# Kernel tuning notes

Measured on AMD Instinct MI355X. Metric: run time of the kernel, lower is better.

The kernel has to match this reference:

```python
import jax, jax.numpy as jnp
import numpy as np
import math

D_K = 64

def setup_inputs() -> dict:
    key = jax.random.key(0)
    k1, k2, k3, k4 = jax.random.split(key, 4)
    B, H, S, D = 2, 16, 2048, D_K
    query = jax.random.normal(k1, (B, H, S, D), dtype=jnp.float32)
    kk = jax.random.normal(k2, (B, H, S, D), dtype=jnp.float32)
    value = jax.random.normal(k3, (B, H, S, D), dtype=jnp.float32)
    mask = jax.random.randint(k4, (B, 1, S, S), 0, 2).astype(bool)
    return {"query": query, "key": kk, "value": value, "mask": mask}

def reference(query, key, value, mask):
    # score = Q K^T / sqrt(d_k)  -> [B,H,S,S]
    score = jnp.einsum('bhqd,bhkd->bhqk', query, key) * (1.0 / math.sqrt(D_K))
    # masked_fill(mask, -inf)
    score = jnp.where(mask, -jnp.inf, score)
    attn = jax.nn.softmax(score, axis=-1)
    # rows that are fully masked produce NaN -> 0 (torch.nan_to_num)
    attn = jnp.nan_to_num(attn, nan=0.0)
    # dropout with drop_rate=0 is identity
    return jnp.einsum('bhqk,bhkd->bhqd', attn, value)
```

## Files before the change

kernel.cpp:

```cpp
#include <hip/hip_runtime.h>
#include <hip/hip_bf16.h>


#define S_LEN 2048
#define D_DIM 64
#define BH    32
#define BM    64
#define BN    64
#define NW    4
#define LDK   72
#define QSCALE 0.1803368801f

typedef __bf16 bf16_t;
typedef bf16_t bf16x8 __attribute__((ext_vector_type(8)));
typedef float  f32x4  __attribute__((ext_vector_type(4)));
typedef unsigned short u16;
typedef unsigned char  u8;
typedef unsigned long long u64b;

template<int CTRL>
__device__ __forceinline__ float dppmov(float v) {
    return __builtin_bit_cast(float,
        __builtin_amdgcn_update_dpp(0, __builtin_bit_cast(int, v),
                                    CTRL, 0xF, 0xF, true));
}
__device__ __forceinline__ float redsum16(float v) {
    v += dppmov<0xB1>(v);
    v += dppmov<0x4E>(v);
    v += dppmov<0x141>(v);
    v += dppmov<0x140>(v);
    return v;
}

__global__ __launch_bounds__(256)
void mask_to_bits(const unsigned* __restrict__ M, u64b* __restrict__ bm)
{
    const int t = threadIdx.x;
    unsigned p = M[(t * 8179) & ((1 << 21) - 1)];
    const int is_u8 = __syncthreads_or(p > 1u);
    const int id = blockIdx.x * 256 + t;
    u64b w = 0;
    if (is_u8) {
        const uint4* src = (const uint4*)((const u8*)M + (size_t)id * 64);
        #pragma unroll
        for (int g = 0; g < 4; ++g) {
            uint4 x = src[g];
            const unsigned dw[4] = {x.x, x.y, x.z, x.w};
            #pragma unroll
            for (int q = 0; q < 4; ++q) {
                const unsigned v = dw[q];
                const int base = g * 16 + q * 4;
                if (v & 0x000000FFu) w |= 1ull << (base + 0);
                if (v & 0x0000FF00u) w |= 1ull << (base + 1);
                if (v & 0x00FF0000u) w |= 1ull << (base + 2);
                if (v & 0xFF000000u) w |= 1ull << (base + 3);
            }
        }
    } else {
        const uint4* src = (const uint4*)(M + (size_t)id * 64);
        #pragma unroll
        for (int g = 0; g < 16; ++g) {
            uint4 x = src[g];
            if (x.x) w |= 1ull << (g * 4 + 0);
            if (x.y) w |= 1ull << (g * 4 + 1);
            if (x.z) w |= 1ull << (g * 4 + 2);
            if (x.w) w |= 1ull << (g * 4 + 3);
        }
    }
    bm[id] = w;
}

__global__ __launch_bounds__(256)
void k_to_bf16(const float* __restrict__ K, bf16_t* __restrict__ Kb)
{
    const size_t i = ((size_t)blockIdx.x * 256 + threadIdx.x) * 8;
    float4 a = *(const float4*)(K + i);
    float4 b = *(const float4*)(K + i + 4);
    bf16x8 w;
    w[0]=(bf16_t)a.x; w[1]=(bf16_t)a.y; w[2]=(bf16_t)a.z; w[3]=(bf16_t)a.w;
    w[4]=(bf16_t)b.x; w[5]=(bf16_t)b.y; w[6]=(bf16_t)b.z; w[7]=(bf16_t)b.w;
    *(bf16x8*)(Kb + i) = w;
}

__global__ __launch_bounds__(256)
void v_transpose(const float* __restrict__ V, bf16_t* __restrict__ Vt)
{
    __shared__ bf16_t T[128][LDK];
    const int t  = threadIdx.x;
    const int sc = blockIdx.x;
    const int bh = blockIdx.y;
    const float* Vh = V + ((size_t)bh * S_LEN + sc * 128) * D_DIM;
    #pragma unroll
    for (int it = 0; it < 4; ++it) {
        const int row = it * 32 + (t >> 3);
        const int c8  = (t & 7) * 8;
        float4 a = *(const float4*)(Vh + row * D_DIM + c8);
        float4 b = *(const float4*)(Vh + row * D_DIM + c8 + 4);
        bf16_t* d = &T[row][c8];
        d[0]=(bf16_t)a.x; d[1]=(bf16_t)a.y; d[2]=(bf16_t)a.z; d[3]=(bf16_t)a.w;
        d[4]=(bf16_t)b.x; d[5]=(bf16_t)b.y; d[6]=(bf16_t)b.z; d[7]=(bf16_t)b.w;
    }
    __syncthreads();
    bf16_t* out = Vt + ((size_t)bh * D_DIM + (t >> 2)) * S_LEN
                     + (size_t)sc * 128 + (t & 3) * 32;
    #pragma unroll
    for (int g = 0; g < 4; ++g) {
        bf16x8 w;
        #pragma unroll
        for (int j = 0; j < 8; ++j) w[j] = T[(t & 3) * 32 + g * 8 + j][t >> 2];
        *(bf16x8*)(out + g * 8) = w;
    }
}

__global__ __launch_bounds__(256, 4)
void fa_fwd(const float* __restrict__ Q, const float* __restrict__ K,
            const float* __restrict__ V, const void* __restrict__ M,
            const u64b* __restrict__ bm, const bf16_t* __restrict__ Kb,
            const bf16_t* __restrict__ Vt, float* __restrict__ O)
{
    __shared__ __align__(16) bf16_t Klds[BN * LDK];
    __shared__ __align__(16) bf16_t Vtlds[D_DIM * LDK];
    __shared__ __align__(16) bf16_t Plds[NW][16 * LDK];

    const int tid  = threadIdx.x;
    const int wave = tid >> 6;
    const int lane = tid & 63;
    const int quad = lane >> 4;
    const int ln   = lane & 15;

    const int qt = blockIdx.x;
    const int bh = blockIdx.y;
    const int b  = bh >> 4;

    const int qbase = qt * BM + wave * 16;

    const size_t head_off = (size_t)bh * S_LEN * D_DIM;
    const float* Qh = Q + head_off;
    const float* Kh = K + head_off;
    const float* Vh = V + head_off;
    const bf16_t* Kbh = Kb ? (Kb + head_off) : nullptr;
    const bf16_t* Vth = Vt ? (Vt + head_off) : nullptr;
    const u8*  Mb8  = (const u8*)M  + (size_t)b * S_LEN * S_LEN;
    const int* Mb32 = (const int*)M + (size_t)b * S_LEN * S_LEN;

    int mask_is_u8 = 0;
    if (!bm) {
        int probe = ((const int*)M)[(tid * 8179) & ((1 << 21) - 1)];
        mask_is_u8 = __syncthreads_or((unsigned)probe > 1u);
    }

    bf16x8 qfrag[2];
    {
        const float* qrow = Qh + (size_t)(qbase + ln) * D_DIM;
        #pragma unroll
        for (int s = 0; s < 2; ++s) {
            float4 a = *(const float4*)(qrow + s * 32 + quad * 8);
            float4 c = *(const float4*)(qrow + s * 32 + quad * 8 + 4);
            bf16x8 w;
            w[0] = (bf16_t)(a.x * QSCALE); w[1] = (bf16_t)(a.y * QSCALE);
            w[2] = (bf16_t)(a.z * QSCALE); w[3] = (bf16_t)(a.w * QSCALE);
            w[4] = (bf16_t)(c.x * QSCALE); w[5] = (bf16_t)(c.y * QSCALE);
            w[6] = (bf16_t)(c.z * QSCALE); w[7] = (bf16_t)(c.w * QSCALE);
            qfrag[s] = w;
        }
    }

    f32x4 accO[4] = {{0.f,0.f,0.f,0.f},{0.f,0.f,0.f,0.f},
                     {0.f,0.f,0.f,0.f},{0.f,0.f,0.f,0.f}};
    float lpart[4] = {0.f, 0.f, 0.f, 0.f};

    const int srow = tid >> 2;
    const int sgrp = tid & 3;
    const int crow = tid >> 3;
    const int cc8  = (tid & 7) * 8;

    const size_t bmrow_base = ((size_t)b * S_LEN + qbase + quad * 4) * 32;

    for (int kb = 0; kb < S_LEN; kb += BN) {
        __syncthreads();

        if (Kbh) {
            #pragma unroll
            for (int it = 0; it < 2; ++it) {
                const int row = it * 32 + crow;
                bf16x8 wk = *(const bf16x8*)(Kbh + (size_t)(kb + row) * D_DIM + cc8);
                *(bf16x8*)&Klds[row * LDK + cc8] = wk;
                bf16x8 wv = *(const bf16x8*)(Vth + (size_t)row * S_LEN + kb + cc8);
                *(bf16x8*)&Vtlds[row * LDK + cc8] = wv;
            }
        } else {
            const float* kp = Kh + (size_t)(kb + srow) * D_DIM + sgrp * 16;
            #pragma unroll
            for (int h = 0; h < 2; ++h) {
                float4 a = *(const float4*)(kp + h * 8);
                float4 c = *(const float4*)(kp + h * 8 + 4);
                bf16x8 w;
                w[0] = (bf16_t)a.x; w[1] = (bf16_t)a.y;
                w[2] = (bf16_t)a.z; w[3] = (bf16_t)a.w;
                w[4] = (bf16_t)c.x; w[5] = (bf16_t)c.y;
                w[6] = (bf16_t)c.z; w[7] = (bf16_t)c.w;
                *(bf16x8*)&Klds[srow * LDK + sgrp * 16 + h * 8] = w;
            }
            const float* vp = Vh + (size_t)(kb + srow) * D_DIM + sgrp * 16;
            float vv[16];
            #pragma unroll
            for (int g = 0; g < 4; ++g) {
                float4 a = *(const float4*)(vp + g * 4);
                vv[g*4+0] = a.x; vv[g*4+1] = a.y;
                vv[g*4+2] = a.z; vv[g*4+3] = a.w;
            }
            #pragma unroll
            for (int jj = 0; jj < 16; ++jj) {
                const int j = (jj + srow) & 15;
                Vtlds[(sgrp * 16 + j) * LDK + srow] = (bf16_t)vv[j];
            }
        }
        __syncthreads();

        f32x4 Sacc[4] = {{0.f,0.f,0.f,0.f},{0.f,0.f,0.f,0.f},
                         {0.f,0.f,0.f,0.f},{0.f,0.f,0.f,0.f}};
        #pragma unroll
        for (int s = 0; s < 2; ++s) {
            #pragma unroll
            for (int t = 0; t < 4; ++t) {
                bf16x8 bk = *(const bf16x8*)&Klds[(16*t + ln) * LDK + s*32 + quad*8];
                Sacc[t] = __builtin_amdgcn_mfma_f32_16x16x32_bf16(qfrag[s], bk, Sacc[t], 0, 0, 0);
            }
        }

        #pragma unroll
        for (int r = 0; r < 4; ++r) {
            float ps[4];
            if (bm) {
                const u64b w  = bm[bmrow_base + (size_t)r * 32 + (kb >> 6)];
                const u64b wl = w >> ln;
                ps[0] = ( wl        & 1ull) ? 0.f : __builtin_amdgcn_exp2f(Sacc[0][r]);
                ps[1] = ((wl >> 16) & 1ull) ? 0.f : __builtin_amdgcn_exp2f(Sacc[1][r]);
                ps[2] = ((wl >> 32) & 1ull) ? 0.f : __builtin_amdgcn_exp2f(Sacc[2][r]);
                ps[3] = ((wl >> 48) & 1ull) ? 0.f : __builtin_amdgcn_exp2f(Sacc[3][r]);
            } else if (mask_is_u8) {
                const u8* mp = Mb8 + (size_t)(qbase + quad*4 + r) * S_LEN + kb + ln;
                #pragma unroll
                for (int t = 0; t < 4; ++t)
                    ps[t] = mp[16*t] ? 0.f : __builtin_amdgcn_exp2f(Sacc[t][r]);
            } else {
                const int* mp = Mb32 + (size_t)(qbase + quad*4 + r) * S_LEN + kb + ln;
                #pragma unroll
                for (int t = 0; t < 4; ++t)
                    ps[t] = mp[16*t] ? 0.f : __builtin_amdgcn_exp2f(Sacc[t][r]);
            }
            lpart[r] += (ps[0] + ps[1]) + (ps[2] + ps[3]);
            #pragma unroll
            for (int t = 0; t < 4; ++t)
                Plds[wave][(quad*4 + r) * LDK + 16*t + ln] = (bf16_t)ps[t];
        }

        __asm__ volatile("" ::: "memory");

        #pragma unroll
        for (int s2 = 0; s2 < 2; ++s2) {
            bf16x8 pa = *(const bf16x8*)&Plds[wave][ln * LDK + s2*32 + quad*8];
            #pragma unroll
            for (int dt = 0; dt < 4; ++dt) {
                bf16x8 bv = *(const bf16x8*)&Vtlds[(16*dt + ln) * LDK + s2*32 + quad*8];
                accO[dt] = __builtin_amdgcn_mfma_f32_16x16x32_bf16(pa, bv, accO[dt], 0, 0, 0);
            }
        }
    }

    #pragma unroll
    for (int r = 0; r < 4; ++r) {
        const float l = redsum16(lpart[r]);
        const float inv = (l > 0.f) ? 1.f / l : 0.f;
        float* orow = O + head_off + (size_t)(qbase + quad*4 + r) * D_DIM;
        #pragma unroll
        for (int dt = 0; dt < 4; ++dt)
            orow[16*dt + ln] = accO[dt][r] * inv;
    }
}

extern "C" void kernel_launch(void* const* d_in, const int* in_sizes, int n_in,
                              void* d_out, int out_size, void* d_ws, size_t ws_size,
                              hipStream_t stream) {
    (void)in_sizes; (void)n_in; (void)out_size;
    const float* Q = (const float*)d_in[0];
    const float* K = (const float*)d_in[1];
    const float* V = (const float*)d_in[2];
    const void*  M = d_in[3];
    float* O = (float*)d_out;

    const size_t bm_bytes = (size_t)2 * S_LEN * (S_LEN / 64) * 8;
    const size_t kv_elems = (size_t)BH * S_LEN * D_DIM;
    const size_t need_kv  = bm_bytes + 2 * kv_elems * sizeof(bf16_t);

    u64b*   bm = (ws_size >= bm_bytes) ? (u64b*)d_ws : nullptr;
    bf16_t* Kb = nullptr;
    bf16_t* Vt = nullptr;
    if (ws_size >= need_kv) {
        Kb = (bf16_t*)((char*)d_ws + bm_bytes);
        Vt = Kb + kv_elems;
    }

    if (bm)
        mask_to_bits<<<dim3(131072 / 256), dim3(256), 0, stream>>>(
            (const unsigned*)M, bm);
    if (Kb) {
        k_to_bf16<<<dim3((unsigned)(kv_elems / 8 / 256)), dim3(256), 0, stream>>>(K, Kb);
        v_transpose<<<dim3(S_LEN / 128, BH), dim3(256), 0, stream>>>(V, Vt);
    }

    dim3 grid(S_LEN / BM, BH);
    fa_fwd<<<grid, dim3(256), 0, stream>>>(Q, K, V, M, bm, Kb, Vt, O);
}
```

Before: 199.0 us.

## Double-buffer K/V tiles via async global-to-LDS loads with XOR-swizzled layout

```diff
diff --git a/kernel.cpp b/kernel.cpp
--- a/kernel.cpp
+++ b/kernel.cpp
@@ -8,7 +8,7 @@
 #define BM    64
 #define BN    64
 #define NW    4
-#define LDK   72
+#define PST   72
 #define QSCALE 0.1803368801f
 
 typedef __bf16 bf16_t;
@@ -17,6 +17,12 @@
 typedef unsigned short u16;
 typedef unsigned char  u8;
 typedef unsigned long long u64b;
+
+__device__ __forceinline__ void load_lds16(const bf16_t* g, bf16_t* l) {
+    __builtin_amdgcn_global_load_lds(
+        (const __attribute__((address_space(1))) void*)g,
+        (__attribute__((address_space(3))) void*)l, 16, 0, 0);
+}
 
 template<int CTRL>
 __device__ __forceinline__ float dppmov(float v) {
@@ -71,21 +77,36 @@
 }
 
 __global__ __launch_bounds__(256)
-void k_to_bf16(const float* __restrict__ K, bf16_t* __restrict__ Kb)
+void qk_prep(const float* __restrict__ Q, const float* __restrict__ K,
+             bf16_t* __restrict__ Qb, bf16_t* __restrict__ Kb)
 {
     const size_t i = ((size_t)blockIdx.x * 256 + threadIdx.x) * 8;
-    float4 a = *(const float4*)(K + i);
-    float4 b = *(const float4*)(K + i + 4);
-    bf16x8 w;
-    w[0]=(bf16_t)a.x; w[1]=(bf16_t)a.y; w[2]=(bf16_t)a.z; w[3]=(bf16_t)a.w;
-    w[4]=(bf16_t)b.x; w[5]=(bf16_t)b.y; w[6]=(bf16_t)b.z; w[7]=(bf16_t)b.w;
-    *(bf16x8*)(Kb + i) = w;
+    {
+        float4 a = *(const float4*)(Q + i);
+        float4 b = *(const float4*)(Q + i + 4);
+        bf16x8 w;
+        w[0]=(bf16_t)(a.x*QSCALE); w[1]=(bf16_t)(a.y*QSCALE);
+        w[2]=(bf16_t)(a.z*QSCALE); w[3]=(bf16_t)(a.w*QSCALE);
+        w[4]=(bf16_t)(b.x*QSCALE); w[5]=(bf16_t)(b.y*QSCALE);
+        w[6]=(bf16_t)(b.z*QSCALE); w[7]=(bf16_t)(b.w*QSCALE);
+        *(bf16x8*)(Qb + i) = w;
+    }
+    {
+        float4 a = *(const float4*)(K + i);
+        float4 b = *(const float4*)(K + i + 4);
+        bf16x8 w;
+        w[0]=(bf16_t)a.x; w[1]=(bf16_t)a.y; w[2]=(bf16_t)a.z; w[3]=(bf16_t)a.w;
+        w[4]=(bf16_t)b.x; w[5]=(bf16_t)b.y; w[6]=(bf16_t)b.z; w[7]=(bf16_t)b.w;
+        const size_t r = i >> 6;
+        const int    g = (int)((i & 63) >> 3);
+        *(bf16x8*)(Kb + r * 64 + ((g ^ (int)(r & 7)) * 8)) = w;
+    }
 }
 
 __global__ __launch_bounds__(256)
 void v_transpose(const float* __restrict__ V, bf16_t* __restrict__ Vt)
 {
-    __shared__ bf16_t T[128][LDK];
+    __shared__ bf16_t T[128][PST];
     const int t  = threadIdx.x;
     const int sc = blockIdx.x;
     const int bh = blockIdx.y;
@@ -101,26 +122,33 @@
         d[4]=(bf16_t)b.x; d[5]=(bf16_t)b.y; d[6]=(bf16_t)b.z; d[7]=(bf16_t)b.w;
     }
     __syncthreads();
-    bf16_t* out = Vt + ((size_t)bh * D_DIM + (t >> 2)) * S_LEN
-                     + (size_t)sc * 128 + (t & 3) * 32;
+    const int d = t >> 2;
     #pragma unroll
     for (int g = 0; g < 4; ++g) {
+        const int s_off = (t & 3) * 32 + g * 8;
+        const int kbt   = sc * 2 + (s_off >> 6);
+        const int k_in  = s_off & 63;
+        const int gk    = k_in >> 3;
         bf16x8 w;
         #pragma unroll
-        for (int j = 0; j < 8; ++j) w[j] = T[(t & 3) * 32 + g * 8 + j][t >> 2];
-        *(bf16x8*)(out + g * 8) = w;
-    }
-}
-
-__global__ __launch_bounds__(256, 4)
+        for (int j = 0; j < 8; ++j) w[j] = T[s_off + j][d];
+        *(bf16x8*)(Vt + (((size_t)bh * (S_LEN/BN) + kbt) * D_DIM + d) * 64
+                      + ((gk ^ (d & 7)) * 8)) = w;
+    }
+}
+
+__global__ __launch_bounds__(256, 3)
 void fa_fwd(const float* __restrict__ Q, const float* __restrict__ K,
             const float* __restrict__ V, const void* __restrict__ M,
-            const u64b* __restrict__ bm, const bf16_t* __restrict__ Kb,
-            const bf16_t* __restrict__ Vt, float* __restrict__ O)
+            const u64b* __restrict__ bm, const bf16_t* __restrict__ Qb,
+            const bf16_t* __restrict__ Kb, const bf16_t* __restrict__ Vt,
+            float* __restrict__ O)
 {
-    __shared__ __align__(16) bf16_t Klds[BN * LDK];
-    __shared__ __align__(16) bf16_t Vtlds[D_DIM * LDK];
-    __shared__ __align__(16) bf16_t Plds[NW][16 * LDK];
+    __shared__ __align__(16) bf16_t KldsA[BN * D_DIM];
+    __shared__ __align__(16) bf16_t KldsB[BN * D_DIM];
+    __shared__ __align__(16) bf16_t VldsA[D_DIM * BN];
+    __shared__ __align__(16) bf16_t VldsB[D_DIM * BN];
+    __shared__ __align__(16) bf16_t Plds[NW][16 * PST];
 
     const int tid  = threadIdx.x;
     const int wave = tid >> 6;
@@ -131,7 +159,6 @@
     const int qt = blockIdx.x;
     const int bh = blockIdx.y;
     const int b  = bh >> 4;
-
     const int qbase = qt * BM + wave * 16;
 
     const size_t head_off = (size_t)bh * S_LEN * D_DIM;
@@ -139,7 +166,6 @@
     const float* Kh = K + head_off;
     const float* Vh = V + head_off;
     const bf16_t* Kbh = Kb ? (Kb + head_off) : nullptr;
-    const bf16_t* Vth = Vt ? (Vt + head_off) : nullptr;
     const u8*  Mb8  = (const u8*)M  + (size_t)b * S_LEN * S_LEN;
     const int* Mb32 = (const int*)M + (size_t)b * S_LEN * S_LEN;
 
@@ -150,17 +176,21 @@
     }
 
     bf16x8 qfrag[2];
-    {
+    if (Qb) {
+        const bf16_t* qrow = Qb + head_off + (size_t)(qbase + ln) * D_DIM;
+        qfrag[0] = *(const bf16x8*)(qrow + quad * 8);
+        qfrag[1] = *(const bf16x8*)(qrow + 32 + quad * 8);
+    } else {
         const float* qrow = Qh + (size_t)(qbase + ln) * D_DIM;
         #pragma unroll
         for (int s = 0; s < 2; ++s) {
             float4 a = *(const float4*)(qrow + s * 32 + quad * 8);
             float4 c = *(const float4*)(qrow + s * 32 + quad * 8 + 4);
             bf16x8 w;
-            w[0] = (bf16_t)(a.x * QSCALE); w[1] = (bf16_t)(a.y * QSCALE);
-            w[2] = (bf16_t)(a.z * QSCALE); w[3] = (bf16_t)(a.w * QSCALE);
-            w[4] = (bf16_t)(c.x * QSCALE); w[5] = (bf16_t)(c.y * QSCALE);
-            w[6] = (bf16_t)(c.z * QSCALE); w[7] = (bf16_t)(c.w * QSCALE);
+            w[0]=(bf16_t)(a.x*QSCALE); w[1]=(bf16_t)(a.y*QSCALE);
+            w[2]=(bf16_t)(a.z*QSCALE); w[3]=(bf16_t)(a.w*QSCALE);
+            w[4]=(bf16_t)(c.x*QSCALE); w[5]=(bf16_t)(c.y*QSCALE);
+            w[6]=(bf16_t)(c.z*QSCALE); w[7]=(bf16_t)(c.w*QSCALE);
             qfrag[s] = w;
         }
     }
@@ -169,102 +199,133 @@
                      {0.f,0.f,0.f,0.f},{0.f,0.f,0.f,0.f}};
     float lpart[4] = {0.f, 0.f, 0.f, 0.f};
 
-    const int srow = tid >> 2;
-    const int sgrp = tid & 3;
-    const int crow = tid >> 3;
-    const int cc8  = (tid & 7) * 8;
-
     const size_t bmrow_base = ((size_t)b * S_LEN + qbase + quad * 4) * 32;
-
-    for (int kb = 0; kb < S_LEN; kb += BN) {
-        __syncthreads();
-
-        if (Kbh) {
-            #pragma unroll
-            for (int it = 0; it < 2; ++it) {
-                const int row = it * 32 + crow;
-                bf16x8 wk = *(const bf16x8*)(Kbh + (size_t)(kb + row) * D_DIM + cc8);
-                *(bf16x8*)&Klds[row * LDK + cc8] = wk;
-                bf16x8 wv = *(const bf16x8*)(Vth + (size_t)row * S_LEN + kb + cc8);
-                *(bf16x8*)&Vtlds[row * LDK + cc8] = wv;
+    const int xg = ln & 7;
+
+    auto load_wm = [&](int kb, u64b* wm) {
+        if (bm) {
+            #pragma unroll
+            for (int r = 0; r < 4; ++r)
+                wm[r] = bm[bmrow_base + (size_t)r * 32 + (kb >> 6)];
+        } else if (mask_is_u8) {
+            #pragma unroll
+            for (int r = 0; r < 4; ++r) {
+                const u8* mp = Mb8 + (size_t)(qbase + quad*4 + r) * S_LEN + kb + ln;
+                u64b w = 0;
+                #pragma unroll
+                for (int t = 0; t < 4; ++t)
+                    if (mp[16*t]) w |= 1ull << (16*t + ln);
+                wm[r] = w;
             }
         } else {
+            #pragma unroll
+            for (int r = 0; r < 4; ++r) {
+                const int* mp = Mb32 + (size_t)(qbase + quad*4 + r) * S_LEN + kb + ln;
+                u64b w = 0;
+                #pragma unroll
+                for (int t = 0; t < 4; ++t)
+                    if (mp[16*t]) w |= 1ull << (16*t + ln);
+                wm[r] = w;
+            }
+        }
+    };
+
+    auto prefetch = [&](int kb, bf16_t* Kl, bf16_t* Vl) {
+        const bf16_t* kt = Kbh + (size_t)kb * D_DIM;
+        const bf16_t* vt = Vt + ((size_t)bh * (S_LEN/BN) + (kb >> 6)) * (BN * D_DIM);
+        #pragma unroll
+        for (int i = 0; i < 2; ++i) {
+            const int c = wave + 4 * i;
+            load_lds16(kt + c * 512 + lane * 8, Kl + c * 512);
+            load_lds16(vt + c * 512 + lane * 8, Vl + c * 512);
+        }
+    };
+
+    auto compute_tile = [&](const bf16_t* Kl, const bf16_t* Vl, const u64b* wm) {
+        f32x4 Sacc[4] = {{0.f,0.f,0.f,0.f},{0.f,0.f,0.f,0.f},
+                         {0.f,0.f,0.f,0.f},{0.f,0.f,0.f,0.f}};
+        #pragma unroll
+        for (int s = 0; s < 2; ++s) {
+            #pragma unroll
+            for (int t = 0; t < 4; ++t) {
+                bf16x8 bk = *(const bf16x8*)
+                    &Kl[(16*t + ln) * D_DIM + (((s*4 + quad) ^ xg) * 8)];
+                Sacc[t] = __builtin_amdgcn_mfma_f32_16x16x32_bf16(qfrag[s], bk, Sacc[t], 0, 0, 0);
+            }
+        }
+        #pragma unroll
+        for (int r = 0; r < 4; ++r) {
+            const u64b wl = wm[r] >> ln;
+            float ps[4];
+            ps[0] = ( wl        & 1ull) ? 0.f : __builtin_amdgcn_exp2f(Sacc[0][r]);
+            ps[1] = ((wl >> 16) & 1ull) ? 0.f : __builtin_amdgcn_exp2f(Sacc[1][r]);
+            ps[2] = ((wl >> 32) & 1ull) ? 0.f : __builtin_amdgcn_exp2f(Sacc[2][r]);
+            ps[3] = ((wl >> 48) & 1ull) ? 0.f : __builtin_amdgcn_exp2f(Sacc[3][r]);
+            lpart[r] += (ps[0] + ps[1]) + (ps[2] + ps[3]);
+            #pragma unroll
+            for (int t = 0; t < 4; ++t)
+                Plds[wave][(quad*4 + r) * PST + 16*t + ln] = (bf16_t)ps[t];
+        }
+        __asm__ volatile("" ::: "memory");
+        #pragma unroll
+        for (int s2 = 0; s2 < 2; ++s2) {
+            bf16x8 pa = *(const bf16x8*)&Plds[wave][ln * PST + s2*32 + quad*8];
+            #pragma unroll
+            for (int dt = 0; dt < 4; ++dt) {
+                bf16x8 bv = *(const bf16x8*)
+                    &Vl[(16*dt + ln) * D_DIM + (((s2*4 + quad) ^ xg) * 8)];
+                accO[dt] = __builtin_amdgcn_mfma_f32_16x16x32_bf16(pa, bv, accO[dt], 0, 0, 0);
+            }
+        }
+    };
+
+    if (Kbh) {
+        prefetch(0, KldsA, VldsA);
+        for (int kb = 0; kb < S_LEN; kb += 2 * BN) {
+            u64b wm[4];
+            __syncthreads();
+            load_wm(kb, wm);
+            if (kb + BN < S_LEN) prefetch(kb + BN, KldsB, VldsB);
+            compute_tile(KldsA, VldsA, wm);
+            __syncthreads();
+            load_wm(kb + BN, wm);
+            if (kb + 2*BN < S_LEN) prefetch(kb + 2*BN, KldsA, VldsA);
+            compute_tile(KldsB, VldsB, wm);
+        }
+    } else {
+        const int srow = tid >> 2;
+        const int sgrp = tid & 3;
+        for (int kb = 0; kb < S_LEN; kb += BN) {
+            __syncthreads();
             const float* kp = Kh + (size_t)(kb + srow) * D_DIM + sgrp * 16;
             #pragma unroll
             for (int h = 0; h < 2; ++h) {
                 float4 a = *(const float4*)(kp + h * 8);
                 float4 c = *(const float4*)(kp + h * 8 + 4);
                 bf16x8 w;
-                w[0] = (bf16_t)a.x; w[1] = (bf16_t)a.y;
-                w[2] = (bf16_t)a.z; w[3] = (bf16_t)a.w;
-                w[4] = (bf16_t)c.x; w[5] = (bf16_t)c.y;
-                w[6] = (bf16_t)c.z; w[7] = (bf16_t)c.w;
-                *(bf16x8*)&Klds[srow * LDK + sgrp * 16 + h * 8] = w;
+                w[0]=(bf16_t)a.x; w[1]=(bf16_t)a.y; w[2]=(bf16_t)a.z; w[3]=(bf16_t)a.w;
+                w[4]=(bf16_t)c.x; w[5]=(bf16_t)c.y; w[6]=(bf16_t)c.z; w[7]=(bf16_t)c.w;
+                const int g = sgrp * 2 + h;
+                *(bf16x8*)&KldsA[srow * D_DIM + ((g ^ (srow & 7)) * 8)] = w;
             }
             const float* vp = Vh + (size_t)(kb + srow) * D_DIM + sgrp * 16;
             float vv[16];
             #pragma unroll
             for (int g = 0; g < 4; ++g) {
                 float4 a = *(const float4*)(vp + g * 4);
-                vv[g*4+0] = a.x; vv[g*4+1] = a.y;
-                vv[g*4+2] = a.z; vv[g*4+3] = a.w;
-            }
+                vv[g*4+0]=a.x; vv[g*4+1]=a.y; vv[g*4+2]=a.z; vv[g*4+3]=a.w;
+            }
+            const int gk = srow >> 3;
             #pragma unroll
             for (int jj = 0; jj < 16; ++jj) {
                 const int j = (jj + srow) & 15;
-                Vtlds[(sgrp * 16 + j) * LDK + srow] = (bf16_t)vv[j];
-            }
-        }
-        __syncthreads();
-
-        f32x4 Sacc[4] = {{0.f,0.f,0.f,0.f},{0.f,0.f,0.f,0.f},
-                         {0.f,0.f,0.f,0.f},{0.f,0.f,0.f,0.f}};
-        #pragma unroll
-        for (int s = 0; s < 2; ++s) {
-            #pragma unroll
-            for (int t = 0; t < 4; ++t) {
-                bf16x8 bk = *(const bf16x8*)&Klds[(16*t + ln) * LDK + s*32 + quad*8];
-                Sacc[t] = __builtin_amdgcn_mfma_f32_16x16x32_bf16(qfrag[s], bk, Sacc[t], 0, 0, 0);
-            }
-        }
-
-        #pragma unroll
-        for (int r = 0; r < 4; ++r) {
-            float ps[4];
-            if (bm) {
-                const u64b w  = bm[bmrow_base + (size_t)r * 32 + (kb >> 6)];
-                const u64b wl = w >> ln;
-                ps[0] = ( wl        & 1ull) ? 0.f : __builtin_amdgcn_exp2f(Sacc[0][r]);
-                ps[1] = ((wl >> 16) & 1ull) ? 0.f : __builtin_amdgcn_exp2f(Sacc[1][r]);
-                ps[2] = ((wl >> 32) & 1ull) ? 0.f : __builtin_amdgcn_exp2f(Sacc[2][r]);
-                ps[3] = ((wl >> 48) & 1ull) ? 0.f : __builtin_amdgcn_exp2f(Sacc[3][r]);
-            } else if (mask_is_u8) {
-                const u8* mp = Mb8 + (size_t)(qbase + quad*4 + r) * S_LEN + kb + ln;
-                #pragma unroll
-                for (int t = 0; t < 4; ++t)
-                    ps[t] = mp[16*t] ? 0.f : __builtin_amdgcn_exp2f(Sacc[t][r]);
-            } else {
-                const int* mp = Mb32 + (size_t)(qbase + quad*4 + r) * S_LEN + kb + ln;
-                #pragma unroll
-                for (int t = 0; t < 4; ++t)
-                    ps[t] = mp[16*t] ? 0.f : __builtin_amdgcn_exp2f(Sacc[t][r]);
-            }
-            lpart[r] += (ps[0] + ps[1]) + (ps[2] + ps[3]);
-            #pragma unroll
-            for (int t = 0; t < 4; ++t)
-                Plds[wave][(quad*4 + r) * LDK + 16*t + ln] = (bf16_t)ps[t];
-        }
-
-        __asm__ volatile("" ::: "memory");
-
-        #pragma unroll
-        for (int s2 = 0; s2 < 2; ++s2) {
-            bf16x8 pa = *(const bf16x8*)&Plds[wave][ln * LDK + s2*32 + quad*8];
-            #pragma unroll
-            for (int dt = 0; dt < 4; ++dt) {
-                bf16x8 bv = *(const bf16x8*)&Vtlds[(16*dt + ln) * LDK + s2*32 + quad*8];
-                accO[dt] = __builtin_amdgcn_mfma_f32_16x16x32_bf16(pa, bv, accO[dt], 0, 0, 0);
-            }
+                const int d = sgrp * 16 + j;
+                VldsA[d * D_DIM + ((gk ^ (d & 7)) * 8) + (srow & 7)] = (bf16_t)vv[j];
+            }
+            __syncthreads();
+            u64b wm[4];
+            load_wm(kb, wm);
+            compute_tile(KldsA, VldsA, wm);
         }
     }
 
@@ -291,13 +352,13 @@
 
     const size_t bm_bytes = (size_t)2 * S_LEN * (S_LEN / 64) * 8;
     const size_t kv_elems = (size_t)BH * S_LEN * D_DIM;
-    const size_t need_kv  = bm_bytes + 2 * kv_elems * sizeof(bf16_t);
+    const size_t need_all = bm_bytes + 3 * kv_elems * sizeof(bf16_t);
 
     u64b*   bm = (ws_size >= bm_bytes) ? (u64b*)d_ws : nullptr;
-    bf16_t* Kb = nullptr;
-    bf16_t* Vt = nullptr;
-    if (ws_size >= need_kv) {
-        Kb = (bf16_t*)((char*)d_ws + bm_bytes);
+    bf16_t* Qb = nullptr; bf16_t* Kb = nullptr; bf16_t* Vt = nullptr;
+    if (ws_size >= need_all) {
+        Qb = (bf16_t*)((char*)d_ws + bm_bytes);
+        Kb = Qb + kv_elems;
         Vt = Kb + kv_elems;
     }
 
@@ -305,10 +366,10 @@
         mask_to_bits<<<dim3(131072 / 256), dim3(256), 0, stream>>>(
             (const unsigned*)M, bm);
     if (Kb) {
-        k_to_bf16<<<dim3((unsigned)(kv_elems / 8 / 256)), dim3(256), 0, stream>>>(K, Kb);
+        qk_prep<<<dim3((unsigned)(kv_elems / 8 / 256)), dim3(256), 0, stream>>>(Q, K, Qb, Kb);
         v_transpose<<<dim3(S_LEN / 128, BH), dim3(256), 0, stream>>>(V, Vt);
     }
 
     dim3 grid(S_LEN / BM, BH);
-    fa_fwd<<<grid, dim3(256), 0, stream>>>(Q, K, V, M, bm, Kb, Vt, O);
-}
+    fa_fwd<<<grid, dim3(256), 0, stream>>>(Q, K, V, M, bm, Qb, Kb, Vt, O);
+}
```

Result: no change. 198.4 us (-0.3%).
